# Optimization experiments

Hardware: AMD Instinct MI355X
Metric: run time of the kernel (lower is better)

Reference implementation:

```python
import jax, jax.numpy as jnp
import numpy as np

N_NODES = 100000
N_EDGES = 3200000
NEG_SLOPE = 0.2
EPS = 1e-16


def _gat_layer(x, src, dst, W, att_src, att_dst, bias, heads, out_ch, concat, num_nodes):
    # x: [N, F_in] -> h: [N, H, C]
    h = (x @ W).reshape(num_nodes, heads, out_ch)
    a_src = jnp.einsum('nhc,hc->nh', h, att_src)  # [N, H]
    a_dst = jnp.einsum('nhc,hc->nh', h, att_dst)  # [N, H]
    # edge-wise raw scores with LeakyReLU
    alpha = jax.nn.leaky_relu(a_src[src] + a_dst[dst], NEG_SLOPE)  # [E, H]
    # segment softmax over incoming edges of each destination node
    seg_max = jax.ops.segment_max(alpha, dst, num_segments=num_nodes)  # [N, H]
    alpha = jnp.exp(alpha - seg_max[dst])
    denom = jax.ops.segment_sum(alpha, dst, num_segments=num_nodes)  # [N, H]
    alpha = alpha / (denom[dst] + EPS)  # [E, H]
    # weighted message scatter-add
    msg = h[src] * alpha[:, :, None]  # [E, H, C]
    out = jax.ops.segment_sum(msg, dst, num_segments=num_nodes)  # [N, H, C]
    if concat:
        out = out.reshape(num_nodes, heads * out_ch)
    else:
        out = out.mean(axis=1)
    return out + bias, alpha


def setup_inputs() -> dict:
    key = jax.random.key(0)
    ks = jax.random.split(key, 11)
    x = jax.random.normal(ks[0], (N_NODES, 2), dtype=jnp.float32)
    edge_index = jax.random.randint(ks[1], (2, N_EDGES), 0, N_NODES)
    s = 0.3
    return {
        'x': x,
        'edge_index': edge_index,
        'W1': jax.random.normal(ks[2], (2, 64), dtype=jnp.float32) * s,
        'att_src1': jax.random.normal(ks[3], (8, 8), dtype=jnp.float32) * s,
        'att_dst1': jax.random.normal(ks[4], (8, 8), dtype=jnp.float32) * s,
        'bias1': jnp.zeros((64,), dtype=jnp.float32),
        'W2': jax.random.normal(ks[5], (64, 2), dtype=jnp.float32) * s,
        'att_src2': jax.random.normal(ks[6], (1, 2), dtype=jnp.float32) * s,
        'att_dst2': jax.random.normal(ks[7], (1, 2), dtype=jnp.float32) * s,
        'bias2': jnp.zeros((2,), dtype=jnp.float32),
    }


def reference(x, edge_index, W1, att_src1, att_dst1, bias1, W2, att_src2, att_dst2, bias2):
    num_nodes = x.shape[0]
    # PyG GATConv default add_self_loops=True: append (i, i) for every node
    loop = jnp.arange(num_nodes, dtype=edge_index.dtype)
    src = jnp.concatenate([edge_index[0], loop])
    dst = jnp.concatenate([edge_index[1], loop])
    h1, alpha1 = _gat_layer(x, src, dst, W1, att_src1, att_dst1, bias1,
                            heads=8, out_ch=8, concat=True, num_nodes=num_nodes)
    h1 = jax.nn.elu(h1)
    h2, alpha2 = _gat_layer(h1, src, dst, W2, att_src2, att_dst2, bias2,
                            heads=1, out_ch=2, concat=False, num_nodes=num_nodes)
    return h2, alpha1, alpha2
```

## Files before the change

kernel.cpp:

```cpp
#include <hip/hip_runtime.h>
#include <math.h>


#define N_NODES 100000
#define N_EDGES 3200000
#define E_TOT   (N_EDGES + N_NODES)
#define NEG_SLOPE 0.2f
#define GAT_EPS 1e-16f
#define RCLAMP 80.0f
#define SCAN_NBLK ((N_NODES + 255) / 256)

__device__ __forceinline__ float lrelu(float r) {
    return r > 0.f ? r : NEG_SLOPE * r;
}

__global__ void k_node1(const float* __restrict__ x,
                        const float* __restrict__ W1,
                        const float* __restrict__ as1,
                        const float* __restrict__ ad1,
                        float* __restrict__ asrc,
                        float* __restrict__ adp,
                        int* __restrict__ cnt,
                        int* __restrict__ fill)
{
    int n = blockIdx.x * blockDim.x + threadIdx.x;
    if (n >= N_NODES) return;
    float x0 = x[2*n+0], x1 = x[2*n+1];
    #pragma unroll
    for (int h = 0; h < 8; ++h) {
        float s = 0.f, d = 0.f;
        #pragma unroll
        for (int c = 0; c < 8; ++c) {
            int j = h*8 + c;
            float v = fmaf(x0, W1[j], x1 * W1[64 + j]);
            s = fmaf(v, as1[j], s);
            d = fmaf(v, ad1[j], d);
        }
        asrc[n*8+h] = s;
        adp[(size_t)n*16+h] = d;
    }
    cnt[n] = 0;
    fill[n] = 0;
}

__global__ void k_hist(const int* __restrict__ ei, int* __restrict__ cnt)
{
    int e = blockIdx.x * blockDim.x + threadIdx.x;
    if (e >= E_TOT) return;
    int d = (e < N_EDGES) ? ei[N_EDGES + e] : e - N_EDGES;
    atomicAdd(&cnt[d], 1);
}

__global__ void k_scan_partial(const int* __restrict__ cnt, int* __restrict__ part)
{
    __shared__ int s[256];
    int t = threadIdx.x;
    int i = blockIdx.x * 256 + t;
    s[t] = (i < N_NODES) ? cnt[i] : 0;
    __syncthreads();
    #pragma unroll
    for (int off = 128; off > 0; off >>= 1) {
        if (t < off) s[t] += s[t + off];
        __syncthreads();
    }
    if (t == 0) part[blockIdx.x] = s[0];
}

__global__ void k_scan_single(const int* __restrict__ part, int* __restrict__ partpre)
{
    __shared__ int s[512];
    int t = threadIdx.x;
    int c = (t < SCAN_NBLK) ? part[t] : 0;
    s[t] = c;
    __syncthreads();
    for (int off = 1; off < 512; off <<= 1) {
        int v = (t >= off) ? s[t - off] : 0;
        __syncthreads();
        s[t] += v;
        __syncthreads();
    }
    if (t < SCAN_NBLK) partpre[t] = s[t] - c;
}

__global__ void k_scan_final(const int* __restrict__ cnt,
                             const int* __restrict__ partpre,
                             int* __restrict__ rowstart)
{
    __shared__ int s[256];
    int t = threadIdx.x;
    int i = blockIdx.x * 256 + t;
    int c = (i < N_NODES) ? cnt[i] : 0;
    s[t] = c;
    __syncthreads();
    for (int off = 1; off < 256; off <<= 1) {
        int v = (t >= off) ? s[t - off] : 0;
        __syncthreads();
        s[t] += v;
        __syncthreads();
    }
    if (i < N_NODES) rowstart[i] = partpre[blockIdx.x] + s[t] - c;
}

__global__ void k_fill(const int* __restrict__ ei,
                       const int* __restrict__ rowstart,
                       int* __restrict__ fill,
                       int* __restrict__ csr_src)
{
    int e = blockIdx.x * blockDim.x + threadIdx.x;
    if (e >= E_TOT) return;
    int s, d;
    if (e < N_EDGES) { s = ei[e]; d = ei[N_EDGES + e]; } else { s = d = e - N_EDGES; }
    int pos = rowstart[d] + atomicAdd(&fill[d], 1);
    csr_src[pos] = s;
}

__global__ void __launch_bounds__(256) k_gat1(
        const int* __restrict__ rowstart,
        const int* __restrict__ cnt,
        const int* __restrict__ csr_src,
        const float* __restrict__ x,
        const float* __restrict__ W1,
        const float* __restrict__ asrc1,
        float* __restrict__ adp,
        const float* __restrict__ b1,
        const float* __restrict__ W2,
        const float* __restrict__ as2,
        const float* __restrict__ ad2,
        float4* __restrict__ nd2,
        float* __restrict__ asrc2)
{
    int wave = threadIdx.x >> 6;
    int lane = threadIdx.x & 63;
    int n = blockIdx.x * 4 + wave;
    if (n >= N_NODES) return;
    int h = lane & 7;
    int j = lane >> 3;

    float adst_h = adp[(size_t)n*16 + h];
    int start = rowstart[n];
    int deg   = cnt[n];
    const float2* x2 = (const float2*)x;

    int idx = j;
    int sP = csr_src[start + min(idx, deg-1)];
    float  aP = asrc1[(size_t)sP*8 + h];
    float2 xP = x2[sP];

    float den = 0.f, S0 = 0.f, S1 = 0.f;
    int iters = (deg + 7) >> 3;
    for (int i = 0; i < iters; ++i) {
        float a = aP; float2 xs = xP;
        int curIdx = idx;
        idx += 8;
        int cl = min(idx, deg-1);
        sP = csr_src[start + cl];
        aP = asrc1[(size_t)sP*8 + h];
        xP = x2[sP];
        float r = fminf(lrelu(a + adst_h), RCLAMP);
        float p = (curIdx < deg) ? __expf(r) : 0.f;
        den += p;
        S0 = fmaf(p, xs.x, S0);
        S1 = fmaf(p, xs.y, S1);
    }
    #pragma unroll
    for (int off = 8; off <= 32; off <<= 1) {
        den += __shfl_xor(den, off, 64);
        S0  += __shfl_xor(S0,  off, 64);
        S1  += __shfl_xor(S1,  off, 64);
    }
    float invden = 1.f / (den + GAT_EPS);
    if (j == 0) adp[(size_t)n*16 + 8 + h] = invden;

    int cI = h*8 + j;
    float w0 = W1[cI], w1 = W1[64 + cI];
    float v = fmaf(w0, S0, w1 * S1) * invden + b1[cI];
    v = v > 0.f ? v : expm1f(v);
    float c0 = v * W2[2*cI+0];
    float c1 = v * W2[2*cI+1];
    #pragma unroll
    for (int off = 1; off <= 32; off <<= 1) {
        c0 += __shfl_xor(c0, off, 64);
        c1 += __shfl_xor(c1, off, 64);
    }
    if (lane == 0) {
        float s2 = fmaf(c0, as2[0], c1 * as2[1]);
        float d2 = fmaf(c0, ad2[0], c1 * ad2[1]);
        nd2[n] = make_float4(c0, c1, s2, d2);
        asrc2[n] = s2;
    }
}

__global__ void __launch_bounds__(256) k_gat2(
        const int* __restrict__ rowstart,
        const int* __restrict__ cnt,
        const int* __restrict__ csr_src,
        const float4* __restrict__ nd2,
        const float* __restrict__ b2,
        float* __restrict__ out_h2,
        float2* __restrict__ pk2)
{
    int t = threadIdx.x & 15;
    int n = blockIdx.x * 16 + (threadIdx.x >> 4);
    if (n >= N_NODES) return;
    float ad = nd2[n].w;
    int start = rowstart[n];
    int deg   = cnt[n];

    int idx = t;
    float4 qP = nd2[csr_src[start + min(idx, deg-1)]];

    float den = 0.f, a0 = 0.f, a1 = 0.f;
    int iters = (deg + 15) >> 4;
    for (int i = 0; i < iters; ++i) {
        float4 q = qP;
        int curIdx = idx;
        idx += 16;
        qP = nd2[csr_src[start + min(idx, deg-1)]];
        float r = fminf(lrelu(q.z + ad), RCLAMP);
        float p = (curIdx < deg) ? __expf(r) : 0.f;
        den += p;
        a0 = fmaf(p, q.x, a0);
        a1 = fmaf(p, q.y, a1);
    }
    #pragma unroll
    for (int off = 1; off <= 8; off <<= 1) {
        den += __shfl_xor(den, off, 64);
        a0  += __shfl_xor(a0,  off, 64);
        a1  += __shfl_xor(a1,  off, 64);
    }
    float invden = 1.f / (den + GAT_EPS);
    if (t == 0) {
        out_h2[(size_t)n*2+0] = a0 * invden + b2[0];
        out_h2[(size_t)n*2+1] = a1 * invden + b2[1];
        pk2[n] = make_float2(ad, invden);
    }
}

__global__ void k_alpha(const int* __restrict__ ei,
                        const float* __restrict__ asrc1,
                        const float* __restrict__ adp,
                        const float* __restrict__ asrc2,
                        const float2* __restrict__ pk2,
                        float* __restrict__ out_a1,
                        float* __restrict__ out_a2)
{
    int e = blockIdx.x * blockDim.x + threadIdx.x;
    if (e >= E_TOT) return;
    int s, d;
    if (e < N_EDGES) { s = ei[e]; d = ei[N_EDGES + e]; } else { s = d = e - N_EDGES; }
    const float4* av = (const float4*)(asrc1 + (size_t)s*8);
    const float4* pv = (const float4*)(adp   + (size_t)d*16);
    float4 a0=av[0], a1=av[1];
    float4 b0=pv[0], b1=pv[1], i0=pv[2], i1=pv[3];
    float4 o0, o1;
    o0.x = __expf(fminf(lrelu(a0.x+b0.x), RCLAMP)) * i0.x;
    o0.y = __expf(fminf(lrelu(a0.y+b0.y), RCLAMP)) * i0.y;
    o0.z = __expf(fminf(lrelu(a0.z+b0.z), RCLAMP)) * i0.z;
    o0.w = __expf(fminf(lrelu(a0.w+b0.w), RCLAMP)) * i0.w;
    o1.x = __expf(fminf(lrelu(a1.x+b1.x), RCLAMP)) * i1.x;
    o1.y = __expf(fminf(lrelu(a1.y+b1.y), RCLAMP)) * i1.y;
    o1.z = __expf(fminf(lrelu(a1.z+b1.z), RCLAMP)) * i1.z;
    o1.w = __expf(fminf(lrelu(a1.w+b1.w), RCLAMP)) * i1.w;
    float4* ao = (float4*)(out_a1 + (size_t)e*8);
    ao[0] = o0; ao[1] = o1;

    float2 pk = pk2[d];
    float r = fminf(lrelu(asrc2[s] + pk.x), RCLAMP);
    out_a2[e] = __expf(r) * pk.y;
}

extern "C" void kernel_launch(void* const* d_in, const int* in_sizes, int n_in,
                              void* d_out, int out_size, void* d_ws, size_t ws_size,
                              hipStream_t stream)
{
    const float* x   = (const float*)d_in[0];
    const int*   ei  = (const int*)d_in[1];
    const float* W1  = (const float*)d_in[2];
    const float* as1 = (const float*)d_in[3];
    const float* ad1 = (const float*)d_in[4];
    const float* b1  = (const float*)d_in[5];
    const float* W2  = (const float*)d_in[6];
    const float* as2 = (const float*)d_in[7];
    const float* ad2 = (const float*)d_in[8];
    const float* b2  = (const float*)d_in[9];

    float* out_h2 = (float*)d_out;
    float* out_a1 = out_h2 + (size_t)N_NODES * 2;
    float* out_a2 = out_a1 + (size_t)E_TOT * 8;

    char* ws = (char*)d_ws;
    float4* nd2   = (float4*)ws; ws += (size_t)N_NODES*16;
    float* adp    = (float*)ws;  ws += (size_t)N_NODES*16*4;
    float* asrc1  = (float*)ws;  ws += (size_t)N_NODES*8*4;
    float2* pk2   = (float2*)ws; ws += (size_t)N_NODES*8;
    float* asrc2  = (float*)ws;  ws += (size_t)N_NODES*4;
    int* cnt      = (int*)ws;    ws += (size_t)N_NODES*4;
    int* fill     = (int*)ws;    ws += (size_t)N_NODES*4;
    int* rowstart = (int*)ws;    ws += (size_t)(N_NODES+1)*4;
    int* part     = (int*)ws;    ws += (size_t)512*4;
    int* partpre  = (int*)ws;    ws += (size_t)512*4;
    int* csr_src  = (int*)ws;    ws += (size_t)E_TOT*4;

    dim3 blk(256);
    int gN = (N_NODES + 255) / 256;
    int gE = (E_TOT + 255) / 256;

    k_node1<<<gN, blk, 0, stream>>>(x, W1, as1, ad1, asrc1, adp, cnt, fill);
    k_hist<<<gE, blk, 0, stream>>>(ei, cnt);
    k_scan_partial<<<SCAN_NBLK, blk, 0, stream>>>(cnt, part);
    k_scan_single<<<1, 512, 0, stream>>>(part, partpre);
    k_scan_final<<<SCAN_NBLK, blk, 0, stream>>>(cnt, partpre, rowstart);
    k_fill<<<gE, blk, 0, stream>>>(ei, rowstart, fill, csr_src);
    k_gat1<<<(N_NODES + 3) / 4, blk, 0, stream>>>(rowstart, cnt, csr_src, x, W1,
            asrc1, adp, b1, W2, as2, ad2, nd2, asrc2);
    k_gat2<<<(N_NODES + 15) / 16, blk, 0, stream>>>(rowstart, cnt, csr_src, nd2,
            b2, out_h2, pk2);
    k_alpha<<<gE, blk, 0, stream>>>(ei, asrc1, adp, asrc2, pk2, out_a1, out_a2);
}
```

Baseline: 637.2 us.

## Build CSR via two-pass bucketed fill and pack node attention with features

Replaces the single scatter pass that did a global atomic per destination node with two passes. The first bins edges into 16-node buckets using one atomic per bucket and packs src with the local destination id. The second kernel scatters each bucket into its final CSR position using shared-memory atomics, which should make the global writes more local. It also packs x next to the per-head source attention in a 12-float record, so layer-1 aggregation fetches both from one cache line. The cost is an extra E-sized bins buffer, an extra pass over the edges, and a packed encoding that assumes src fits in 27 bits.

```diff
diff --git a/kernel.cpp b/kernel.cpp
--- a/kernel.cpp
+++ b/kernel.cpp
@@ -5,6 +5,7 @@
 #define N_NODES 100000
 #define N_EDGES 3200000
 #define E_TOT   (N_EDGES + N_NODES)
+#define NBUCK   (N_NODES / 16)
 #define NEG_SLOPE 0.2f
 #define GAT_EPS 1e-16f
 #define RCLAMP 80.0f
@@ -18,10 +19,10 @@
                         const float* __restrict__ W1,
                         const float* __restrict__ as1,
                         const float* __restrict__ ad1,
-                        float* __restrict__ asrc,
+                        float* __restrict__ asp,
                         float* __restrict__ adp,
                         int* __restrict__ cnt,
-                        int* __restrict__ fill)
+                        int* __restrict__ bfill)
 {
     int n = blockIdx.x * blockDim.x + threadIdx.x;
     if (n >= N_NODES) return;
@@ -36,11 +37,13 @@
             s = fmaf(v, as1[j], s);
             d = fmaf(v, ad1[j], d);
         }
-        asrc[n*8+h] = s;
+        asp[(size_t)n*12+h] = s;
         adp[(size_t)n*16+h] = d;
     }
+    asp[(size_t)n*12+8] = x0;
+    asp[(size_t)n*12+9] = x1;
     cnt[n] = 0;
-    fill[n] = 0;
+    if (n < NBUCK) bfill[n] = 0;
 }
 
 __global__ void k_hist(const int* __restrict__ ei, int* __restrict__ cnt)
@@ -101,26 +104,52 @@
     if (i < N_NODES) rowstart[i] = partpre[blockIdx.x] + s[t] - c;
 }
 
-__global__ void k_fill(const int* __restrict__ ei,
-                       const int* __restrict__ rowstart,
-                       int* __restrict__ fill,
-                       int* __restrict__ csr_src)
+__global__ void k_binfill(const int* __restrict__ ei,
+                          const int* __restrict__ rowstart,
+                          int* __restrict__ bfill,
+                          int* __restrict__ bins)
 {
     int e = blockIdx.x * blockDim.x + threadIdx.x;
     if (e >= E_TOT) return;
     int s, d;
     if (e < N_EDGES) { s = ei[e]; d = ei[N_EDGES + e]; } else { s = d = e - N_EDGES; }
-    int pos = rowstart[d] + atomicAdd(&fill[d], 1);
-    csr_src[pos] = s;
+    int b = d >> 4;
+    int base = rowstart[b << 4];
+    int slot = atomicAdd(&bfill[b], 1);
+    bins[base + slot] = (s << 4) | (d & 15);
+}
+
+__global__ void __launch_bounds__(256) k_fill2(
+        const int* __restrict__ bins,
+        const int* __restrict__ rowstart,
+        int* __restrict__ csr_src)
+{
+    __shared__ int lfill[16];
+    __shared__ int lrow[16];
+    int b = blockIdx.x;
+    int t = threadIdx.x;
+    int node0 = b << 4;
+    if (t < 16) {
+        lfill[t] = 0;
+        lrow[t] = rowstart[node0 + t];
+    }
+    __syncthreads();
+    int base = lrow[0];
+    int end = (node0 + 16 < N_NODES) ? rowstart[node0 + 16] : E_TOT;
+    for (int i = base + t; i < end; i += 256) {
+        int v = bins[i];
+        int dl = v & 15;
+        int pos = lrow[dl] + atomicAdd(&lfill[dl], 1);
+        csr_src[pos] = v >> 4;
+    }
 }
 
 __global__ void __launch_bounds__(256) k_gat1(
         const int* __restrict__ rowstart,
         const int* __restrict__ cnt,
         const int* __restrict__ csr_src,
-        const float* __restrict__ x,
+        const float* __restrict__ asp,
         const float* __restrict__ W1,
-        const float* __restrict__ asrc1,
         float* __restrict__ adp,
         const float* __restrict__ b1,
         const float* __restrict__ W2,
@@ -139,12 +168,11 @@
     float adst_h = adp[(size_t)n*16 + h];
     int start = rowstart[n];
     int deg   = cnt[n];
-    const float2* x2 = (const float2*)x;
 
     int idx = j;
     int sP = csr_src[start + min(idx, deg-1)];
-    float  aP = asrc1[(size_t)sP*8 + h];
-    float2 xP = x2[sP];
+    float  aP = asp[(size_t)sP*12 + h];
+    float2 xP = *(const float2*)(asp + (size_t)sP*12 + 8);
 
     float den = 0.f, S0 = 0.f, S1 = 0.f;
     int iters = (deg + 7) >> 3;
@@ -154,8 +182,8 @@
         idx += 8;
         int cl = min(idx, deg-1);
         sP = csr_src[start + cl];
-        aP = asrc1[(size_t)sP*8 + h];
-        xP = x2[sP];
+        aP = asp[(size_t)sP*12 + h];
+        xP = *(const float2*)(asp + (size_t)sP*12 + 8);
         float r = fminf(lrelu(a + adst_h), RCLAMP);
         float p = (curIdx < deg) ? __expf(r) : 0.f;
         den += p;
@@ -237,7 +265,7 @@
 }
 
 __global__ void k_alpha(const int* __restrict__ ei,
-                        const float* __restrict__ asrc1,
+                        const float* __restrict__ asp,
                         const float* __restrict__ adp,
                         const float* __restrict__ asrc2,
                         const float2* __restrict__ pk2,
@@ -248,8 +276,8 @@
     if (e >= E_TOT) return;
     int s, d;
     if (e < N_EDGES) { s = ei[e]; d = ei[N_EDGES + e]; } else { s = d = e - N_EDGES; }
-    const float4* av = (const float4*)(asrc1 + (size_t)s*8);
-    const float4* pv = (const float4*)(adp   + (size_t)d*16);
+    const float4* av = (const float4*)(asp + (size_t)s*12);
+    const float4* pv = (const float4*)(adp + (size_t)d*16);
     float4 a0=av[0], a1=av[1];
     float4 b0=pv[0], b1=pv[1], i0=pv[2], i1=pv[3];
     float4 o0, o1;
@@ -290,12 +318,13 @@
 
     char* ws = (char*)d_ws;
     float4* nd2   = (float4*)ws; ws += (size_t)N_NODES*16;
+    int* bins     = (int*)ws;    ws += (size_t)E_TOT*4;
+    float* asp    = (float*)ws;  ws += (size_t)N_NODES*12*4;
     float* adp    = (float*)ws;  ws += (size_t)N_NODES*16*4;
-    float* asrc1  = (float*)ws;  ws += (size_t)N_NODES*8*4;
     float2* pk2   = (float2*)ws; ws += (size_t)N_NODES*8;
     float* asrc2  = (float*)ws;  ws += (size_t)N_NODES*4;
     int* cnt      = (int*)ws;    ws += (size_t)N_NODES*4;
-    int* fill     = (int*)ws;    ws += (size_t)N_NODES*4;
+    int* bfill    = (int*)ws;    ws += (size_t)NBUCK*4;
     int* rowstart = (int*)ws;    ws += (size_t)(N_NODES+1)*4;
     int* part     = (int*)ws;    ws += (size_t)512*4;
     int* partpre  = (int*)ws;    ws += (size_t)512*4;
@@ -305,15 +334,16 @@
     int gN = (N_NODES + 255) / 256;
     int gE = (E_TOT + 255) / 256;
 
-    k_node1<<<gN, blk, 0, stream>>>(x, W1, as1, ad1, asrc1, adp, cnt, fill);
+    k_node1<<<gN, blk, 0, stream>>>(x, W1, as1, ad1, asp, adp, cnt, bfill);
     k_hist<<<gE, blk, 0, stream>>>(ei, cnt);
     k_scan_partial<<<SCAN_NBLK, blk, 0, stream>>>(cnt, part);
     k_scan_single<<<1, 512, 0, stream>>>(part, partpre);
     k_scan_final<<<SCAN_NBLK, blk, 0, stream>>>(cnt, partpre, rowstart);
-    k_fill<<<gE, blk, 0, stream>>>(ei, rowstart, fill, csr_src);
-    k_gat1<<<(N_NODES + 3) / 4, blk, 0, stream>>>(rowstart, cnt, csr_src, x, W1,
-            asrc1, adp, b1, W2, as2, ad2, nd2, asrc2);
+    k_binfill<<<gE, blk, 0, stream>>>(ei, rowstart, bfill, bins);
+    k_fill2<<<NBUCK, blk, 0, stream>>>(bins, rowstart, csr_src);
+    k_gat1<<<(N_NODES + 3) / 4, blk, 0, stream>>>(rowstart, cnt, csr_src, asp,
+            W1, adp, b1, W2, as2, ad2, nd2, asrc2);
     k_gat2<<<(N_NODES + 15) / 16, blk, 0, stream>>>(rowstart, cnt, csr_src, nd2,
             b2, out_h2, pk2);
-    k_alpha<<<gE, blk, 0, stream>>>(ei, asrc1, adp, asrc2, pk2, out_a1, out_a2);
-}
+    k_alpha<<<gE, blk, 0, stream>>>(ei, asp, adp, asrc2, pk2, out_a1, out_a2);
+}
```

New measurement: 704.5 us. 1.11x slower.
